# Optimization experiments

Measured on AMD Instinct MI355X. Metric: run time of the kernel, lower is better.

Reference implementation:

```python
import jax, jax.numpy as jnp
import numpy as np

B, E, N1, K, CIN, CB, COUT, G = 2, 2048, 96, 32, 64, 32, 64, 4
NEG_SLOPE = 0.01  # nn.LeakyReLU default


def setup_inputs() -> dict:
    key = jax.random.key(0)
    ks = jax.random.split(key, 9)
    sites1 = jax.random.normal(ks[0], (B, N1, CIN), jnp.float32)
    sites2 = jax.random.normal(ks[1], (B, K, CIN), jnp.float32)
    bonds = jax.random.normal(ks[2], (B, E, CB), jnp.float32)
    idx1 = jax.random.randint(ks[3], (E,), 0, N1, jnp.int32)
    idx2 = jax.random.randint(ks[4], (E,), 0, K, jnp.int32)
    idx2_oh = jax.nn.one_hot(idx2, K, dtype=jnp.float32)  # [E, K]
    F = 2 * CIN + CB
    W_eq = jax.random.normal(ks[5], (G, F, COUT), jnp.float32) / np.float32(np.sqrt(F))
    b_eq = jnp.zeros((COUT,), jnp.float32)
    W_att = jax.random.normal(ks[6], (COUT, 1), jnp.float32) / np.float32(np.sqrt(COUT))
    b_att = jnp.zeros((1,), jnp.float32)
    # permutation group action on the K cells: identity + random perms
    perms = [jnp.arange(K, dtype=jnp.int32)]
    pk = ks[7]
    for _ in range(G - 1):
        pk, sk = jax.random.split(pk)
        perms.append(jax.random.permutation(sk, K).astype(jnp.int32))
    perms1 = jnp.stack(perms)  # [G, K]
    perms2 = perms1            # same action on input and output cell axes
    return dict(sites1=sites1, sites2=sites2, bonds=bonds, W_eq=W_eq, b_eq=b_eq,
                W_att=W_att, b_att=b_att, idx2_oh=idx2_oh, idx1=idx1, idx2=idx2,
                perms1=perms1, perms2=perms2)


def reference(sites1, sites2, bonds, W_eq, b_eq, W_att, b_att, idx2_oh, idx1, idx2, perms1, perms2):
    Bn = sites1.shape[0]
    Gn, Kn = perms1.shape
    On = W_eq.shape[2]
    # gather sender / receiver site features along the site axis
    sites_s = jnp.take(sites1, idx1, axis=1)              # [B,E,CIN]
    sites_r = jnp.take(sites2, idx2, axis=1)              # [B,E,CIN]
    vectors = jnp.concatenate([sites_s, sites_r, bonds], axis=2)  # [B,E,F]
    # outer-product expansion onto cells (idx2_oh is one-hot over K)
    vc = jnp.einsum('bef,ek->befk', vectors, idx2_oh)     # [B,E,F,K]
    # permutation-equivariant linear (group-averaged): per-group-element weight,
    # input cells permuted by perms1, output cells un-permuted by perms2
    xg = vc[:, :, :, perms1]                               # [B,E,F,G,K]
    yg = jnp.einsum('befgk,gfo->beogk', xg, W_eq)          # [B,E,O,G,K]
    inv2 = jnp.argsort(perms2, axis=1)                     # inverse perms [G,K]
    garr = jnp.arange(Gn)[:, None]
    y = yg[:, :, :, garr, inv2].mean(axis=3)               # [B,E,O,K]
    y = jax.nn.leaky_relu(y + b_eq[None, None, :, None], NEG_SLOPE)
    # gather each edge's receiving cell slot == dot with one-hot
    lat = jnp.einsum('beok,ek->beo', y, idx2_oh)           # [B,E,O]
    att = jax.nn.sigmoid(jnp.einsum('beo,oj->bej', lat, W_att) + b_att)  # [B,E,1]
    lat = att * lat
    # scatter_add over edges into receiving sites
    out = jnp.zeros((Bn, Kn, On), lat.dtype).at[:, idx2].add(lat)  # [B,K,O]
    return out
```

## Files before the change

kernel.cpp:

```cpp
#include <hip/hip_runtime.h>
#include <math.h>

#define Bn   2
#define En   2048
#define N1n  96
#define Kn   32
#define CINn 64
#define CBn  32
#define On   64
#define Gn   4
#define Fn   160
#define NEG  0.01f
#define NW   8
#define NT   (NW * 64)
#define EB   8

__global__ void __launch_bounds__(NT, 1)
fused_kernel(const float* __restrict__ sites1, const float* __restrict__ sites2,
             const float* __restrict__ bonds,  const float* __restrict__ W_eq,
             const float* __restrict__ b_eq,   const float* __restrict__ W_att,
             const float* __restrict__ b_att,  const int* __restrict__ idx1,
             const int* __restrict__ idx2,     const int* __restrict__ perms1,
             const int* __restrict__ perms2,   float* __restrict__ out) {
    __shared__ float Weff[Fn][On];
    __shared__ float vs[NW][EB][96];
    __shared__ float red[NW][On];
    __shared__ float s2[CINn];
    __shared__ float wgs[Gn];
    __shared__ int   elist[En];
    __shared__ int   ecount;

    const int t  = threadIdx.x;
    const int bk = blockIdx.x;
    const int b  = bk >> 5;
    const int k2 = bk & (Kn - 1);

    if (t < Gn) {
        int g = t, j = 0;
        for (; j < Kn; ++j) if (perms2[g * Kn + j] == k2) break;
        wgs[g] = (j < Kn && perms1[g * Kn + j] == k2) ? 1.f : 0.f;
    }
    if (t == Gn) ecount = 0;
    __syncthreads();

    {
        const float w0 = wgs[0], w1 = wgs[1], w2 = wgs[2], w3 = wgs[3];
        const float4* W4 = (const float4*)W_eq;
        float4* Wd = (float4*)&Weff[0][0];
        const int n4 = Fn * On / 4;
        for (int i = t; i < n4; i += NT) {
            float4 a0 = W4[i], a1 = W4[n4 + i], a2 = W4[2 * n4 + i], a3 = W4[3 * n4 + i];
            float4 r;
            r.x = 0.25f * (w0 * a0.x + w1 * a1.x + w2 * a2.x + w3 * a3.x);
            r.y = 0.25f * (w0 * a0.y + w1 * a1.y + w2 * a2.y + w3 * a3.y);
            r.z = 0.25f * (w0 * a0.z + w1 * a1.z + w2 * a2.z + w3 * a3.z);
            r.w = 0.25f * (w0 * a0.w + w1 * a1.w + w2 * a2.w + w3 * a3.w);
            Wd[i] = r;
        }
    }

    for (int e = t; e < En; e += NT)
        if (idx2[e] == k2) { int p = atomicAdd(&ecount, 1); elist[p] = e; }

    if (t < CINn) s2[t] = sites2[(b * Kn + k2) * CINn + t];
    __syncthreads();

    const int w    = t >> 6;
    const int lane = t & 63;
    const int og   = lane & 15;
    const int fg   = lane >> 4;
    const int ec   = ecount;

    const float4 be4 = ((const float4*)b_eq)[og];
    const float4 wa  = ((const float4*)W_att)[og];
    const float  ba  = b_att[0];

    float4 p2 = make_float4(0.f, 0.f, 0.f, 0.f);
#pragma unroll
    for (int fi = 0; fi < 16; ++fi) {
        const int f  = 64 + 4 * fi + fg;
        const float  vf = s2[4 * fi + fg];
        const float4 wv = *(const float4*)&Weff[f][og * 4];
        p2.x += vf * wv.x; p2.y += vf * wv.y;
        p2.z += vf * wv.z; p2.w += vf * wv.w;
    }

    float4 oacc = make_float4(0.f, 0.f, 0.f, 0.f);

    for (int base = w * EB; base < ec; base += NW * EB) {
        const int nb = (ec - base < EB) ? (ec - base) : EB;

        __builtin_amdgcn_wave_barrier();
#pragma unroll
        for (int j = 0; j < EB; ++j) {
            const int jj = j < nb ? j : nb - 1;
            const int e  = elist[base + jj];
            const int i1 = idx1[e];
            vs[w][j][lane] = sites1[((b * N1n + i1) << 6) + lane];
            if (lane < CBn) vs[w][j][CINn + lane] = bonds[(b * En + e) * CBn + lane];
        }
        __builtin_amdgcn_wave_barrier();

        float4 acc[EB];
#pragma unroll
        for (int j = 0; j < EB; ++j) acc[j] = p2;

#pragma unroll
        for (int fi = 0; fi < 24; ++fi) {
            const int vsidx = 4 * fi + fg;
            const int f     = vsidx < CINn ? vsidx : vsidx + CINn;
            const float4 wv = *(const float4*)&Weff[f][og * 4];
#pragma unroll
            for (int j = 0; j < EB; ++j) {
                const float vf = vs[w][j][vsidx];
                acc[j].x += vf * wv.x; acc[j].y += vf * wv.y;
                acc[j].z += vf * wv.z; acc[j].w += vf * wv.w;
            }
        }
        __builtin_amdgcn_wave_barrier();

#pragma unroll
        for (int j = 0; j < EB; ++j) {
            float4 a = acc[j];
#pragma unroll
            for (int m = 16; m <= 32; m <<= 1) {
                a.x += __shfl_xor(a.x, m);
                a.y += __shfl_xor(a.y, m);
                a.z += __shfl_xor(a.z, m);
                a.w += __shfl_xor(a.w, m);
            }
            float4 lat;
            lat.x = a.x + be4.x; lat.x = lat.x > 0.f ? lat.x : NEG * lat.x;
            lat.y = a.y + be4.y; lat.y = lat.y > 0.f ? lat.y : NEG * lat.y;
            lat.z = a.z + be4.z; lat.z = lat.z > 0.f ? lat.z : NEG * lat.z;
            lat.w = a.w + be4.w; lat.w = lat.w > 0.f ? lat.w : NEG * lat.w;

            float part = lat.x * wa.x + lat.y * wa.y + lat.z * wa.z + lat.w * wa.w;
#pragma unroll
            for (int m = 1; m <= 8; m <<= 1) part += __shfl_xor(part, m);

            float att = 1.f / (1.f + expf(-(part + ba)));
            att *= (j < nb) ? 1.f : 0.f;
            oacc.x += att * lat.x;
            oacc.y += att * lat.y;
            oacc.z += att * lat.z;
            oacc.w += att * lat.w;
        }
    }

    if (fg == 0) *(float4*)&red[w][og * 4] = oacc;
    __syncthreads();

    if (t < On) {
        float s = 0.f;
#pragma unroll
        for (int q = 0; q < NW; ++q) s += red[q][t];
        out[((size_t)b * Kn + k2) * On + t] = s;
    }
}

extern "C" void kernel_launch(void* const* d_in, const int* in_sizes, int n_in,
                              void* d_out, int out_size, void* d_ws, size_t ws_size,
                              hipStream_t stream) {
    const float* sites1 = (const float*)d_in[0];
    const float* sites2 = (const float*)d_in[1];
    const float* bonds  = (const float*)d_in[2];
    const float* W_eq   = (const float*)d_in[3];
    const float* b_eq   = (const float*)d_in[4];
    const float* W_att  = (const float*)d_in[5];
    const float* b_att  = (const float*)d_in[6];
    const int*   idx1   = (const int*)d_in[8];
    const int*   idx2   = (const int*)d_in[9];
    const int*   perms1 = (const int*)d_in[10];
    const int*   perms2 = (const int*)d_in[11];
    float* out = (float*)d_out;

    fused_kernel<<<Bn * Kn, NT, 0, stream>>>(
        sites1, sites2, bonds, W_eq, b_eq, W_att, b_att,
        idx1, idx2, perms1, perms2, out);
}
```

Before: 98.93 us.

## Split each receiver bucket across four blocks and reduce partials in a second kernel

Each (batch, receiving cell) bucket is now processed by four blocks, each handling the edges whose index falls in one residue class mod 4, so the grid grows from 64 to 256 blocks to fill more compute units. The per-wave edge batch is shrunk to match the smaller per-block edge count, and the shared edge list is capped at 256 entries. Partial sums go to a workspace, and a separate small kernel adds the four partials into the output. This adds a kernel launch and redundant per-block weight-mixing and index scanning, and it relies on no sub-bucket exceeding the list cap.

Result: faster. 86.46 us (-12.6%).

```diff
diff --git a/kernel.cpp b/kernel.cpp
--- a/kernel.cpp
+++ b/kernel.cpp
@@ -13,7 +13,9 @@
 #define NEG  0.01f
 #define NW   8
 #define NT   (NW * 64)
-#define EB   8
+#define EB   2
+#define SUBn 4
+#define ELCAP 256
 
 __global__ void __launch_bounds__(NT, 1)
 fused_kernel(const float* __restrict__ sites1, const float* __restrict__ sites2,
@@ -21,19 +23,20 @@
              const float* __restrict__ b_eq,   const float* __restrict__ W_att,
              const float* __restrict__ b_att,  const int* __restrict__ idx1,
              const int* __restrict__ idx2,     const int* __restrict__ perms1,
-             const int* __restrict__ perms2,   float* __restrict__ out) {
+             const int* __restrict__ perms2,   float* __restrict__ ws) {
     __shared__ float Weff[Fn][On];
     __shared__ float vs[NW][EB][96];
     __shared__ float red[NW][On];
     __shared__ float s2[CINn];
     __shared__ float wgs[Gn];
-    __shared__ int   elist[En];
+    __shared__ int   elist[ELCAP];
     __shared__ int   ecount;
 
-    const int t  = threadIdx.x;
-    const int bk = blockIdx.x;
-    const int b  = bk >> 5;
-    const int k2 = bk & (Kn - 1);
+    const int t      = threadIdx.x;
+    const int bucket = blockIdx.x >> 2;
+    const int sub    = blockIdx.x & (SUBn - 1);
+    const int b      = bucket >> 5;
+    const int k2     = bucket & (Kn - 1);
 
     if (t < Gn) {
         int g = t, j = 0;
@@ -48,6 +51,7 @@
         const float4* W4 = (const float4*)W_eq;
         float4* Wd = (float4*)&Weff[0][0];
         const int n4 = Fn * On / 4;
+#pragma unroll
         for (int i = t; i < n4; i += NT) {
             float4 a0 = W4[i], a1 = W4[n4 + i], a2 = W4[2 * n4 + i], a3 = W4[3 * n4 + i];
             float4 r;
@@ -60,7 +64,10 @@
     }
 
     for (int e = t; e < En; e += NT)
-        if (idx2[e] == k2) { int p = atomicAdd(&ecount, 1); elist[p] = e; }
+        if (idx2[e] == k2 && (e & (SUBn - 1)) == sub) {
+            int p = atomicAdd(&ecount, 1);
+            elist[p] = e;
+        }
 
     if (t < CINn) s2[t] = sites2[(b * Kn + k2) * CINn + t];
     __syncthreads();
@@ -155,8 +162,17 @@
         float s = 0.f;
 #pragma unroll
         for (int q = 0; q < NW; ++q) s += red[q][t];
-        out[((size_t)b * Kn + k2) * On + t] = s;
+        ws[((size_t)bucket * SUBn + sub) * On + t] = s;
     }
+}
+
+__global__ void __launch_bounds__(256)
+reduce_kernel(const float* __restrict__ ws, float* __restrict__ out) {
+    const int i = blockIdx.x * 256 + threadIdx.x;
+    const int bucket = i >> 6;
+    const int o      = i & (On - 1);
+    const float* p = ws + (size_t)bucket * SUBn * On + o;
+    out[i] = (p[0] + p[On]) + (p[2 * On] + p[3 * On]);
 }
 
 extern "C" void kernel_launch(void* const* d_in, const int* in_sizes, int n_in,
@@ -174,8 +190,10 @@
     const int*   perms1 = (const int*)d_in[10];
     const int*   perms2 = (const int*)d_in[11];
     float* out = (float*)d_out;
+    float* ws  = (float*)d_ws;
 
-    fused_kernel<<<Bn * Kn, NT, 0, stream>>>(
+    fused_kernel<<<Bn * Kn * SUBn, NT, 0, stream>>>(
         sites1, sites2, bonds, W_eq, b_eq, W_att, b_att,
-        idx1, idx2, perms1, perms2, out);
+        idx1, idx2, perms1, perms2, ws);
+    reduce_kernel<<<(Bn * Kn * On) / 256, 256, 0, stream>>>(ws, out);
 }
```
